# Kernel optimization log

Hardware: AMD Instinct MI355X
Metric: run time of the kernel (lower is better)

## Reference

```python
import jax, jax.numpy as jnp
import numpy as np

DIM = 1024
HEADS = 16
HEAD_DIM = DIM // HEADS
EPS = 1e-5


def layer_norm(x, w, b):
    # normalize over last dim (head_dim)
    mu = jnp.mean(x, axis=-1, keepdims=True)
    var = jnp.mean(jnp.square(x - mu), axis=-1, keepdims=True)
    return (x - mu) * jax.lax.rsqrt(var + EPS) * w + b


def setup_inputs() -> dict:
    key = jax.random.key(0)
    ks = jax.random.split(key, 8)
    B, N = 2, 2048
    x = jax.random.normal(ks[0], (B, N, DIM), dtype=jnp.float32)
    mask = jax.random.randint(ks[1], (B, 1, N, N), 0, 2) == 1  # True = masked out
    qkv_w = jax.random.normal(ks[2], (3 * DIM, DIM), dtype=jnp.float32) * (DIM ** -0.5)
    q_norm_w = jnp.ones((HEAD_DIM,), dtype=jnp.float32)
    q_norm_b = jnp.zeros((HEAD_DIM,), dtype=jnp.float32)
    k_norm_w = jnp.ones((HEAD_DIM,), dtype=jnp.float32)
    k_norm_b = jnp.zeros((HEAD_DIM,), dtype=jnp.float32)
    proj_w = jax.random.normal(ks[3], (DIM, DIM), dtype=jnp.float32) * (DIM ** -0.5)
    proj_b = jnp.zeros((DIM,), dtype=jnp.float32)
    return {"x": x, "mask": mask, "qkv_w": qkv_w,
            "q_norm_w": q_norm_w, "q_norm_b": q_norm_b,
            "k_norm_w": k_norm_w, "k_norm_b": k_norm_b,
            "proj_w": proj_w, "proj_b": proj_b}


def reference(x, mask, qkv_w, q_norm_w, q_norm_b, k_norm_w, k_norm_b, proj_w, proj_b):
    B, N, C = x.shape
    H, D = HEADS, HEAD_DIM
    scale = D ** -0.5
    # qkv projection (no bias), split into q,k,v of shape (B,H,N,D)
    qkv = (x @ qkv_w.T).reshape(B, N, 3, H, D).transpose(2, 0, 3, 1, 4)
    q, k, v = qkv[0], qkv[1], qkv[2]
    q = layer_norm(q, q_norm_w, q_norm_b)
    k = layer_norm(k, k_norm_w, k_norm_b)
    q = q * scale
    attn = jnp.einsum("bhnd,bhmd->bhnm", q, k)  # (B,H,N,N)
    attn = jnp.where(mask, -jnp.inf, attn)
    attn = jax.nn.softmax(attn, axis=-1)
    out = jnp.einsum("bhnm,bhmd->bhnd", attn, v)
    out = out.transpose(0, 2, 1, 3).reshape(B, N, C)
    return out @ proj_w.T + proj_b
```

## Files before the change

### kernel.cpp

```cpp
#include <hip/hip_runtime.h>
#include <hip/hip_bf16.h>
#include <math.h>

#define B_    2
#define N_    2048
#define DIM_  1024
#define H_    16
#define HD_   64
#define EPS_  1e-5f
#define SCALE_ 0.125f
#define LOG2E_ 1.4426950408889634f
#define MFIX_  14.0f

typedef __attribute__((ext_vector_type(8))) __bf16 bf16x8;
typedef __attribute__((ext_vector_type(8))) unsigned short ushort8;
typedef __attribute__((ext_vector_type(4))) float f32x4;
typedef __attribute__((ext_vector_type(4))) unsigned int uint4v;

__device__ __forceinline__ unsigned short f2bf(float x) {
    unsigned u = __builtin_bit_cast(unsigned, x);
    u += 0x7fff + ((u >> 16) & 1);
    return (unsigned short)(u >> 16);
}
__device__ __forceinline__ unsigned pk2bf(float a, float b) {
    unsigned ua = __builtin_bit_cast(unsigned, a) + 0x8000u;
    unsigned ub = __builtin_bit_cast(unsigned, b) + 0x8000u;
    return __builtin_amdgcn_perm(ub, ua, 0x07060302);
}

__device__ __forceinline__ void gl_lds16(const void* g, void* l) {
    __builtin_amdgcn_global_load_lds(
        (const __attribute__((address_space(1))) void*)g,
        (__attribute__((address_space(3))) void*)l, 16, 0, 0);
}

__global__ __launch_bounds__(256) void cast_all_bf16(
    const float* __restrict__ x, const float* __restrict__ qkvw,
    const float* __restrict__ pw, unsigned short* __restrict__ out) {
    int i = (blockIdx.x * 256 + threadIdx.x) * 8;
    const float* src;
    if (i < 4194304) src = x + i;
    else if (i < 7340032) src = qkvw + (i - 4194304);
    else src = pw + (i - 7340032);
    float4 v0 = *(const float4*)src;
    float4 v1 = *(const float4*)(src + 4);
    ushort8 r;
    r[0] = f2bf(v0.x); r[1] = f2bf(v0.y); r[2] = f2bf(v0.z); r[3] = f2bf(v0.w);
    r[4] = f2bf(v1.x); r[5] = f2bf(v1.y); r[6] = f2bf(v1.z); r[7] = f2bf(v1.w);
    *(ushort8*)(out + i) = r;
}

__global__ __launch_bounds__(256) void pack_mask(
    const int* __restrict__ mask, unsigned long long* __restrict__ bm) {
    int w = blockIdx.x * 4 + (threadIdx.x >> 6);
    int lane = threadIdx.x & 63;
    int mv = mask[(size_t)w * 64 + lane];
    unsigned long long bits = __ballot(mv != 0);
    if (lane == 0) bm[w] = bits;
}

__global__ __launch_bounds__(256) void gemm_qkv_ln(
    const unsigned short* __restrict__ A, const unsigned short* __restrict__ Bw,
    const float* __restrict__ qnw, const float* __restrict__ qnb,
    const float* __restrict__ knw, const float* __restrict__ knb,
    unsigned short* __restrict__ qbuf, unsigned short* __restrict__ kbuf,
    unsigned short* __restrict__ vbuf) {
    const int K = DIM_;
    __shared__ unsigned short As[128 * 32];
    __shared__ unsigned short Bs[128 * 32];
    const int tid = threadIdx.x;
    const int wave = tid >> 6, lane = tid & 63;
    const int quad = lane >> 4, lcol = lane & 15;
    const int wr = wave >> 1, wc = wave & 1;
    const int row0 = blockIdx.y * 128, col0 = blockIdx.x * 128;

    f32x4 acc[4][4];
#pragma unroll
    for (int i = 0; i < 4; ++i)
#pragma unroll
        for (int j = 0; j < 4; ++j) acc[i][j] = (f32x4){0.f, 0.f, 0.f, 0.f};

    for (int k0 = 0; k0 < K; k0 += 32) {
        __syncthreads();
#pragma unroll
        for (int c = 0; c < 2; ++c) {
            int base = wave * 2048 + c * 1024;
            int myofs = base + lane * 16;
            int r = myofs >> 6;
            int kb = myofs & 63;
            gl_lds16((const char*)A + ((size_t)(row0 + r) * K + k0) * 2 + kb,
                     (char*)As + base);
            gl_lds16((const char*)Bw + ((size_t)(col0 + r) * K + k0) * 2 + kb,
                     (char*)Bs + base);
        }
        __syncthreads();

        bf16x8 af[4], bfr[4];
#pragma unroll
        for (int i = 0; i < 4; ++i) {
            af[i] = *(const bf16x8*)&As[(wr * 64 + i * 16 + lcol) * 32 + quad * 8];
            bfr[i] = *(const bf16x8*)&Bs[(wc * 64 + i * 16 + lcol) * 32 + quad * 8];
        }
#pragma unroll
        for (int i = 0; i < 4; ++i)
#pragma unroll
            for (int j = 0; j < 4; ++j)
                acc[i][j] = __builtin_amdgcn_mfma_f32_16x16x32_bf16(
                    af[i], bfr[j], acc[i][j], 0, 0, 0);
    }

    const int colbase = col0 + wc * 64;
    const int t = colbase >> 10;
    const int h = (colbase & 1023) >> 6;

    if (t < 2) {
        const float* wv = (t == 0) ? qnw : knw;
        const float* bv = (t == 0) ? qnb : knb;
        float wreg[4], breg[4];
#pragma unroll
        for (int j = 0; j < 4; ++j) {
            wreg[j] = wv[j * 16 + lcol];
            breg[j] = bv[j * 16 + lcol];
        }
        const float sc = (t == 0) ? (SCALE_ * LOG2E_) : 1.f;
        unsigned short* obase = (t == 0) ? qbuf : kbuf;
#pragma unroll
        for (int i = 0; i < 4; ++i) {
#pragma unroll
            for (int reg = 0; reg < 4; ++reg) {
                int row = row0 + wr * 64 + i * 16 + quad * 4 + reg;
                int bb = row >> 11, n = row & (N_ - 1);
                float v[4];
#pragma unroll
                for (int j = 0; j < 4; ++j) v[j] = acc[i][j][reg];
                float s = v[0] + v[1] + v[2] + v[3];
                s += __shfl_xor(s, 1);
                s += __shfl_xor(s, 2);
                s += __shfl_xor(s, 4);
                s += __shfl_xor(s, 8);
                float mu = s * (1.f / 64.f);
                float d[4], s2 = 0.f;
#pragma unroll
                for (int j = 0; j < 4; ++j) {
                    d[j] = v[j] - mu;
                    s2 += d[j] * d[j];
                }
                s2 += __shfl_xor(s2, 1);
                s2 += __shfl_xor(s2, 2);
                s2 += __shfl_xor(s2, 4);
                s2 += __shfl_xor(s2, 8);
                float r = rsqrtf(s2 * (1.f / 64.f) + EPS_);
                float o0 = (d[0] * r * wreg[0] + breg[0]) * sc;
                float o1 = (d[1] * r * wreg[1] + breg[1]) * sc;
                float o2 = (d[2] * r * wreg[2] + breg[2]) * sc;
                float o3 = (d[3] * r * wreg[3] + breg[3]) * sc;
                uint2 pk;
                pk.x = pk2bf(o0, o1);
                pk.y = pk2bf(o2, o3);
                *(uint2*)(obase + ((size_t)(bb * H_ + h) * N_ + n) * 64 +
                          lcol * 4) = pk;
            }
        }
    } else {
#pragma unroll
        for (int i = 0; i < 4; ++i) {
#pragma unroll
            for (int reg = 0; reg < 4; ++reg) {
                int row = row0 + wr * 64 + i * 16 + quad * 4 + reg;
                uint2 pk;
                pk.x = pk2bf(acc[i][0][reg], acc[i][1][reg]);
                pk.y = pk2bf(acc[i][2][reg], acc[i][3][reg]);
                *(uint2*)(vbuf + (size_t)row * DIM_ + h * 64 + lcol * 4) = pk;
            }
        }
    }
}

__global__ __launch_bounds__(256) void gemm_proj(
    const unsigned short* __restrict__ A, const unsigned short* __restrict__ Bw,
    const float* __restrict__ bias, float* __restrict__ Cout) {
    const int K = DIM_;
    __shared__ unsigned short As[128 * 32];
    __shared__ unsigned short Bs[64 * 32];
    const int tid = threadIdx.x;
    const int wave = tid >> 6, lane = tid & 63;
    const int quad = lane >> 4, lcol = lane & 15;
    const int row0 = blockIdx.y * 128, col0 = blockIdx.x * 64;

    f32x4 acc[2][4];
#pragma unroll
    for (int i = 0; i < 2; ++i)
#pragma unroll
        for (int j = 0; j < 4; ++j) acc[i][j] = (f32x4){0.f, 0.f, 0.f, 0.f};

    for (int k0 = 0; k0 < K; k0 += 32) {
        __syncthreads();
#pragma unroll
        for (int pi = 0; pi < 3; ++pi) {
            int p = wave * 3 + pi;
            if (p < 8) {
                int base = p * 1024;
                int myofs = base + lane * 16;
                int r = myofs >> 6, kb = myofs & 63;
                gl_lds16((const char*)A + ((size_t)(row0 + r) * K + k0) * 2 + kb,
                         (char*)As + base);
            } else {
                int base = (p - 8) * 1024;
                int myofs = base + lane * 16;
                int r = myofs >> 6, kb = myofs & 63;
                gl_lds16((const char*)Bw + ((size_t)(col0 + r) * K + k0) * 2 + kb,
                         (char*)Bs + base);
            }
        }
        __syncthreads();

        bf16x8 af[2], bfr[4];
#pragma unroll
        for (int i = 0; i < 2; ++i)
            af[i] = *(const bf16x8*)&As[(wave * 32 + i * 16 + lcol) * 32 + quad * 8];
#pragma unroll
        for (int j = 0; j < 4; ++j)
            bfr[j] = *(const bf16x8*)&Bs[(j * 16 + lcol) * 32 + quad * 8];
#pragma unroll
        for (int i = 0; i < 2; ++i)
#pragma unroll
            for (int j = 0; j < 4; ++j)
                acc[i][j] = __builtin_amdgcn_mfma_f32_16x16x32_bf16(
                    af[i], bfr[j], acc[i][j], 0, 0, 0);
    }

#pragma unroll
    for (int i = 0; i < 2; ++i) {
#pragma unroll
        for (int j = 0; j < 4; ++j) {
            int col = col0 + j * 16 + lcol;
            float bv = bias[col];
#pragma unroll
            for (int reg = 0; reg < 4; ++reg) {
                int row = row0 + wave * 32 + i * 16 + quad * 4 + reg;
                Cout[(size_t)row * DIM_ + col] = acc[i][j][reg] + bv;
            }
        }
    }
}

__global__ __launch_bounds__(256) void transpose_v(
    const unsigned short* __restrict__ vbuf, unsigned short* __restrict__ vt) {
    __shared__ unsigned short Ts[64 * 65];
    const int tid = threadIdx.x;
    const int bh = blockIdx.y, n0 = blockIdx.x * 64;
    const int b = bh >> 4, h = bh & 15;
    {
        int r = tid >> 2, s = tid & 3;
        const unsigned short* src =
            vbuf + (size_t)(b * N_ + n0 + r) * DIM_ + h * 64 + s * 16;
#pragma unroll
        for (int i = 0; i < 16; ++i) {
            int p = s * 16 + i;
            int trued = (p >> 2) + (p & 3) * 16;
            Ts[r * 65 + trued] = src[i];
        }
    }
    __syncthreads();
    {
        int d = tid >> 2, kt = tid & 3;
        unsigned short* dstrow = vt + (size_t)(bh * 64 + d) * N_ + n0;
        int P = kt >> 1, t = kt & 1;
#pragma unroll
        for (int q = 0; q < 4; ++q) {
            __align__(8) unsigned short tmp4[4];
#pragma unroll
            for (int j = 0; j < 4; ++j)
                tmp4[j] = Ts[(kt * 16 + q * 4 + j) * 65 + d];
            *(uint2*)(dstrow + P * 32 + q * 8 + t * 4) = *(const uint2*)tmp4;
        }
    }
}

__global__ __launch_bounds__(256) void flash_attn_mfma6(
    const unsigned short* __restrict__ q, const unsigned short* __restrict__ k,
    const unsigned short* __restrict__ vt,
    const unsigned long long* __restrict__ bm, unsigned short* __restrict__ ao) {
    __shared__ unsigned short Qs[64 * 64];
    __shared__ unsigned short Ks[2][64 * 64];
    __shared__ unsigned short Vts[2][64 * 64];

    const int tid = threadIdx.x;
    const int wave = tid >> 6, lane = tid & 63;
    const int quad = lane >> 4, lcol = lane & 15;
    const int bh = blockIdx.y, b = bh >> 4, h = bh & 15;
    const int q0 = blockIdx.x * 64;

    const char* kgbase = (const char*)k + (size_t)bh * N_ * 128;
    const char* vtbase = (const char*)vt + (size_t)bh * 64 * N_ * 2;

    const char* kp[2];
    const char* vp[2];
#pragma unroll
    for (int ci = 0; ci < 2; ++ci) {
        int c = wave * 2 + ci;
        int swz = (c & 3) * 2;
        kp[ci] = kgbase + (size_t)(lane ^ swz) * 128 + c * 16;
        vp[ci] = vtbase + (size_t)(lane ^ swz) * N_ * 2 + c * 16;
    }

    {
        const char* qg = (const char*)(q + (size_t)(bh * N_ + q0) * 64);
#pragma unroll
        for (int c = 0; c < 2; ++c) {
            int base = wave * 2048 + c * 1024;
            gl_lds16(qg + base + lane * 16, (char*)Qs + base);
        }
#pragma unroll
        for (int ci = 0; ci < 2; ++ci) {
            int c = wave * 2 + ci;
            gl_lds16(kp[ci], (char*)Ks[0] + c * 1024);
            gl_lds16(vp[ci], (char*)Vts[0] + c * 1024);
            kp[ci] += 64 * 128;
            vp[ci] += 64 * 2;
        }
    }
    const unsigned long long* bmq =
        bm + ((size_t)b * N_ + q0 + wave * 16 + lcol) * 32;
    unsigned long long mw_next = bmq[0];
    __syncthreads();

    bf16x8 bq[2];
#pragma unroll
    for (int d0 = 0; d0 < 2; ++d0)
        bq[d0] = *(const bf16x8*)&Qs[(wave * 16 + lcol) * 64 + d0 * 32 + quad * 8];

    ushort8 ot;
#pragma unroll
    for (int i = 0; i < 8; ++i) ot[i] = 0x3F80;
    const bf16x8 ones = __builtin_bit_cast(bf16x8, ot);

    f32x4 oacc[4];
#pragma unroll
    for (int dt = 0; dt < 4; ++dt) oacc[dt] = (f32x4){0.f, 0.f, 0.f, 0.f};
    f32x4 lacc = (f32x4){0.f, 0.f, 0.f, 0.f};

    for (int k0 = 0; k0 < N_; k0 += 64) {
        const int cur = (k0 >> 6) & 1;
        const unsigned long long mw = mw_next;
        if (k0 + 64 < N_) {
#pragma unroll
            for (int ci = 0; ci < 2; ++ci) {
                int c = wave * 2 + ci;
                gl_lds16(kp[ci], (char*)Ks[cur ^ 1] + c * 1024);
                gl_lds16(vp[ci], (char*)Vts[cur ^ 1] + c * 1024);
                kp[ci] += 64 * 128;
                vp[ci] += 64 * 2;
            }
            mw_next = bmq[(k0 >> 6) + 1];
        }

        unsigned long long mq = mw >> (quad * 4);
        unsigned mlo = (unsigned)mq, mhi = (unsigned)(mq >> 32);
        f32x4 sacc[4];
#pragma unroll
        for (int kt = 0; kt < 4; ++kt) {
            unsigned word = (kt < 2) ? mlo : mhi;
            const int sh = (kt & 1) * 16;
#pragma unroll
            for (int reg = 0; reg < 4; ++reg)
                sacc[kt][reg] = ((word >> (sh + reg)) & 1u) ? -1e4f : -MFIX_;
        }

        const char* ksb = (const char*)Ks[cur];
        const char* vsb = (const char*)Vts[cur];
#pragma unroll
        for (int kt = 0; kt < 4; ++kt) {
#pragma unroll
            for (int d0 = 0; d0 < 2; ++d0) {
                int p = d0 * 4 + quad;
                bf16x8 ak = *(const bf16x8*)(ksb + p * 1024 +
                                             (((kt * 16 + lcol) ^ (quad * 2)) << 4));
                sacc[kt] = __builtin_amdgcn_mfma_f32_16x16x32_bf16(
                    ak, bq[d0], sacc[kt], 0, 0, 0);
            }
        }

        uint2 pk[4];
#pragma unroll
        for (int kt = 0; kt < 4; ++kt) {
            float p0 = exp2f(sacc[kt][0]);
            float p1 = exp2f(sacc[kt][1]);
            float p2 = exp2f(sacc[kt][2]);
            float p3 = exp2f(sacc[kt][3]);
            pk[kt].x = pk2bf(p0, p1);
            pk[kt].y = pk2bf(p2, p3);
        }

#pragma unroll
        for (int P = 0; P < 2; ++P) {
            uint4v bu;
            bu[0] = pk[2 * P].x;
            bu[1] = pk[2 * P].y;
            bu[2] = pk[2 * P + 1].x;
            bu[3] = pk[2 * P + 1].y;
            bf16x8 bp = __builtin_bit_cast(bf16x8, bu);
            lacc = __builtin_amdgcn_mfma_f32_16x16x32_bf16(ones, bp, lacc,
                                                           0, 0, 0);
#pragma unroll
            for (int dt = 0; dt < 4; ++dt) {
                int c = P * 4 + quad;
                bf16x8 va = *(const bf16x8*)(vsb + c * 1024 +
                                             (((dt * 16 + lcol) ^ (quad * 2)) << 4));
                oacc[dt] = __builtin_amdgcn_mfma_f32_16x16x32_bf16(
                    va, bp, oacc[dt], 0, 0, 0);
            }
        }
        __syncthreads();
    }

    float inv = 1.f / lacc[0];
    int row = q0 + wave * 16 + lcol;
    unsigned short* dst = ao + ((size_t)(b * N_ + row)) * DIM_ + h * 64 + quad * 4;
#pragma unroll
    for (int dt = 0; dt < 4; ++dt) {
        uint2 pko;
        pko.x = pk2bf(oacc[dt][0] * inv, oacc[dt][1] * inv);
        pko.y = pk2bf(oacc[dt][2] * inv, oacc[dt][3] * inv);
        *(uint2*)(dst + dt * 16) = pko;
    }
}

extern "C" void kernel_launch(void* const* d_in, const int* in_sizes, int n_in,
                              void* d_out, int out_size, void* d_ws,
                              size_t ws_size, hipStream_t stream) {
    const float* x     = (const float*)d_in[0];
    const int*   mask  = (const int*)d_in[1];
    const float* qkv_w = (const float*)d_in[2];
    const float* qnw   = (const float*)d_in[3];
    const float* qnb   = (const float*)d_in[4];
    const float* knw   = (const float*)d_in[5];
    const float* knb   = (const float*)d_in[6];
    const float* pw    = (const float*)d_in[7];
    const float* pb    = (const float*)d_in[8];
    float* out = (float*)d_out;

    char* ws = (char*)d_ws;
    unsigned short* x_bf  = (unsigned short*)(ws + 0);
    unsigned short* qw_bf = (unsigned short*)(ws + 8388608);
    unsigned short* pw_bf = (unsigned short*)(ws + 14680064);
    unsigned short* qbuf  = (unsigned short*)(ws + 16777216);
    unsigned short* kbuf  = (unsigned short*)(ws + 25165824);
    unsigned short* vbuf  = (unsigned short*)(ws + 33554432);
    unsigned short* vt    = (unsigned short*)(ws + 41943040);
    unsigned long long* bmask = (unsigned long long*)(ws + 50331648);
    unsigned short* ao_bnc = vbuf;

    cast_all_bf16<<<8388608 / 2048, 256, 0, stream>>>(x, qkv_w, pw, x_bf);

    gemm_qkv_ln<<<dim3(3072 / 128, 4096 / 128), 256, 0, stream>>>(
        x_bf, qw_bf, qnw, qnb, knw, knb, qbuf, kbuf, vbuf);

    transpose_v<<<dim3(N_ / 64, B_ * H_), 256, 0, stream>>>(vbuf, vt);

    pack_mask<<<(B_ * N_ * (N_ / 64)) / 4, 256, 0, stream>>>(mask, bmask);

    flash_attn_mfma6<<<dim3(N_ / 64, B_ * H_), 256, 0, stream>>>(
        qbuf, kbuf, vt, bmask, ao_bnc);

    gemm_proj<<<dim3(DIM_ / 64, 4096 / 128), 256, 0, stream>>>(
        ao_bnc, pw_bf, pb, out);
}
```

Measured before the change: 290.7 us.

## Process two query fragments per wave in flash attention to reuse K/V tiles

Each attention block now covers 128 query rows instead of 64, with each wave computing two 16-row query fragments against the same K and V tiles read from shared memory. This halves the number of K/V tile loads per query row and the block count, and doubles MFMA work per shared-memory read. In exchange it uses more registers per thread and launches only 512 blocks, which lowers parallelism across the chip's compute units.

Result: faster. 278.3 us (-4.2%).

```diff
diff --git a/kernel.cpp b/kernel.cpp
--- a/kernel.cpp
+++ b/kernel.cpp
@@ -277,11 +277,11 @@
     }
 }
 
-__global__ __launch_bounds__(256) void flash_attn_mfma6(
+__global__ __launch_bounds__(256, 2) void flash_attn_mfma7(
     const unsigned short* __restrict__ q, const unsigned short* __restrict__ k,
     const unsigned short* __restrict__ vt,
     const unsigned long long* __restrict__ bm, unsigned short* __restrict__ ao) {
-    __shared__ unsigned short Qs[64 * 64];
+    __shared__ unsigned short Qs[128 * 64];
     __shared__ unsigned short Ks[2][64 * 64];
     __shared__ unsigned short Vts[2][64 * 64];
 
@@ -289,7 +289,7 @@
     const int wave = tid >> 6, lane = tid & 63;
     const int quad = lane >> 4, lcol = lane & 15;
     const int bh = blockIdx.y, b = bh >> 4, h = bh & 15;
-    const int q0 = blockIdx.x * 64;
+    const int q0 = blockIdx.x * 128;
 
     const char* kgbase = (const char*)k + (size_t)bh * N_ * 128;
     const char* vtbase = (const char*)vt + (size_t)bh * 64 * N_ * 2;
@@ -307,8 +307,8 @@
     {
         const char* qg = (const char*)(q + (size_t)(bh * N_ + q0) * 64);
 #pragma unroll
-        for (int c = 0; c < 2; ++c) {
-            int base = wave * 2048 + c * 1024;
+        for (int c = 0; c < 4; ++c) {
+            int base = wave * 4096 + c * 1024;
             gl_lds16(qg + base + lane * 16, (char*)Qs + base);
         }
 #pragma unroll
@@ -320,29 +320,39 @@
             vp[ci] += 64 * 2;
         }
     }
-    const unsigned long long* bmq =
-        bm + ((size_t)b * N_ + q0 + wave * 16 + lcol) * 32;
-    unsigned long long mw_next = bmq[0];
+    const unsigned long long* bmq0 =
+        bm + ((size_t)b * N_ + q0 + wave * 32 + lcol) * 32;
+    const unsigned long long* bmq1 = bmq0 + 16 * 32;
+    unsigned long long mw_next0 = bmq0[0];
+    unsigned long long mw_next1 = bmq1[0];
     __syncthreads();
 
-    bf16x8 bq[2];
-#pragma unroll
-    for (int d0 = 0; d0 < 2; ++d0)
-        bq[d0] = *(const bf16x8*)&Qs[(wave * 16 + lcol) * 64 + d0 * 32 + quad * 8];
+    bf16x8 bq[2][2];
+#pragma unroll
+    for (int qf = 0; qf < 2; ++qf)
+#pragma unroll
+        for (int d0 = 0; d0 < 2; ++d0)
+            bq[qf][d0] = *(const bf16x8*)&Qs[(wave * 32 + qf * 16 + lcol) * 64 +
+                                             d0 * 32 + quad * 8];
 
     ushort8 ot;
 #pragma unroll
     for (int i = 0; i < 8; ++i) ot[i] = 0x3F80;
     const bf16x8 ones = __builtin_bit_cast(bf16x8, ot);
 
-    f32x4 oacc[4];
-#pragma unroll
-    for (int dt = 0; dt < 4; ++dt) oacc[dt] = (f32x4){0.f, 0.f, 0.f, 0.f};
-    f32x4 lacc = (f32x4){0.f, 0.f, 0.f, 0.f};
+    f32x4 oacc[2][4];
+#pragma unroll
+    for (int qf = 0; qf < 2; ++qf)
+#pragma unroll
+        for (int dt = 0; dt < 4; ++dt) oacc[qf][dt] = (f32x4){0.f, 0.f, 0.f, 0.f};
+    f32x4 lacc[2];
+    lacc[0] = (f32x4){0.f, 0.f, 0.f, 0.f};
+    lacc[1] = (f32x4){0.f, 0.f, 0.f, 0.f};
 
     for (int k0 = 0; k0 < N_; k0 += 64) {
         const int cur = (k0 >> 6) & 1;
-        const unsigned long long mw = mw_next;
+        const unsigned long long mw0 = mw_next0;
+        const unsigned long long mw1 = mw_next1;
         if (k0 + 64 < N_) {
 #pragma unroll
             for (int ci = 0; ci < 2; ++ci) {
@@ -352,19 +362,24 @@
                 kp[ci] += 64 * 128;
                 vp[ci] += 64 * 2;
             }
-            mw_next = bmq[(k0 >> 6) + 1];
-        }
-
-        unsigned long long mq = mw >> (quad * 4);
-        unsigned mlo = (unsigned)mq, mhi = (unsigned)(mq >> 32);
-        f32x4 sacc[4];
-#pragma unroll
-        for (int kt = 0; kt < 4; ++kt) {
-            unsigned word = (kt < 2) ? mlo : mhi;
-            const int sh = (kt & 1) * 16;
-#pragma unroll
-            for (int reg = 0; reg < 4; ++reg)
-                sacc[kt][reg] = ((word >> (sh + reg)) & 1u) ? -1e4f : -MFIX_;
+            mw_next0 = bmq0[(k0 >> 6) + 1];
+            mw_next1 = bmq1[(k0 >> 6) + 1];
+        }
+
+        f32x4 sacc[2][4];
+#pragma unroll
+        for (int qf = 0; qf < 2; ++qf) {
+            unsigned long long mq = ((qf == 0) ? mw0 : mw1) >> (quad * 4);
+            unsigned mlo = (unsigned)mq, mhi = (unsigned)(mq >> 32);
+#pragma unroll
+            for (int kt = 0; kt < 4; ++kt) {
+                unsigned word = (kt < 2) ? mlo : mhi;
+                const int sh = (kt & 1) * 16;
+#pragma unroll
+                for (int reg = 0; reg < 4; ++reg)
+                    sacc[qf][kt][reg] =
+                        ((word >> (sh + reg)) & 1u) ? -1e4f : -MFIX_;
+            }
         }
 
         const char* ksb = (const char*)Ks[cur];
@@ -376,53 +391,68 @@
                 int p = d0 * 4 + quad;
                 bf16x8 ak = *(const bf16x8*)(ksb + p * 1024 +
                                              (((kt * 16 + lcol) ^ (quad * 2)) << 4));
-                sacc[kt] = __builtin_amdgcn_mfma_f32_16x16x32_bf16(
-                    ak, bq[d0], sacc[kt], 0, 0, 0);
-            }
-        }
-
-        uint2 pk[4];
-#pragma unroll
-        for (int kt = 0; kt < 4; ++kt) {
-            float p0 = exp2f(sacc[kt][0]);
-            float p1 = exp2f(sacc[kt][1]);
-            float p2 = exp2f(sacc[kt][2]);
-            float p3 = exp2f(sacc[kt][3]);
-            pk[kt].x = pk2bf(p0, p1);
-            pk[kt].y = pk2bf(p2, p3);
+                sacc[0][kt] = __builtin_amdgcn_mfma_f32_16x16x32_bf16(
+                    ak, bq[0][d0], sacc[0][kt], 0, 0, 0);
+                sacc[1][kt] = __builtin_amdgcn_mfma_f32_16x16x32_bf16(
+                    ak, bq[1][d0], sacc[1][kt], 0, 0, 0);
+            }
+        }
+
+        uint2 pk[2][4];
+#pragma unroll
+        for (int qf = 0; qf < 2; ++qf) {
+#pragma unroll
+            for (int kt = 0; kt < 4; ++kt) {
+                float p0 = exp2f(sacc[qf][kt][0]);
+                float p1 = exp2f(sacc[qf][kt][1]);
+                float p2 = exp2f(sacc[qf][kt][2]);
+                float p3 = exp2f(sacc[qf][kt][3]);
+                pk[qf][kt].x = pk2bf(p0, p1);
+                pk[qf][kt].y = pk2bf(p2, p3);
+            }
         }
 
 #pragma unroll
         for (int P = 0; P < 2; ++P) {
-            uint4v bu;
-            bu[0] = pk[2 * P].x;
-            bu[1] = pk[2 * P].y;
-            bu[2] = pk[2 * P + 1].x;
-            bu[3] = pk[2 * P + 1].y;
-            bf16x8 bp = __builtin_bit_cast(bf16x8, bu);
-            lacc = __builtin_amdgcn_mfma_f32_16x16x32_bf16(ones, bp, lacc,
-                                                           0, 0, 0);
+            bf16x8 bp[2];
+#pragma unroll
+            for (int qf = 0; qf < 2; ++qf) {
+                uint4v bu;
+                bu[0] = pk[qf][2 * P].x;
+                bu[1] = pk[qf][2 * P].y;
+                bu[2] = pk[qf][2 * P + 1].x;
+                bu[3] = pk[qf][2 * P + 1].y;
+                bp[qf] = __builtin_bit_cast(bf16x8, bu);
+                lacc[qf] = __builtin_amdgcn_mfma_f32_16x16x32_bf16(
+                    ones, bp[qf], lacc[qf], 0, 0, 0);
+            }
 #pragma unroll
             for (int dt = 0; dt < 4; ++dt) {
                 int c = P * 4 + quad;
                 bf16x8 va = *(const bf16x8*)(vsb + c * 1024 +
                                              (((dt * 16 + lcol) ^ (quad * 2)) << 4));
-                oacc[dt] = __builtin_amdgcn_mfma_f32_16x16x32_bf16(
-                    va, bp, oacc[dt], 0, 0, 0);
+                oacc[0][dt] = __builtin_amdgcn_mfma_f32_16x16x32_bf16(
+                    va, bp[0], oacc[0][dt], 0, 0, 0);
+                oacc[1][dt] = __builtin_amdgcn_mfma_f32_16x16x32_bf16(
+                    va, bp[1], oacc[1][dt], 0, 0, 0);
             }
         }
         __syncthreads();
     }
 
-    float inv = 1.f / lacc[0];
-    int row = q0 + wave * 16 + lcol;
-    unsigned short* dst = ao + ((size_t)(b * N_ + row)) * DIM_ + h * 64 + quad * 4;
-#pragma unroll
-    for (int dt = 0; dt < 4; ++dt) {
-        uint2 pko;
-        pko.x = pk2bf(oacc[dt][0] * inv, oacc[dt][1] * inv);
-        pko.y = pk2bf(oacc[dt][2] * inv, oacc[dt][3] * inv);
-        *(uint2*)(dst + dt * 16) = pko;
+#pragma unroll
+    for (int qf = 0; qf < 2; ++qf) {
+        float inv = 1.f / lacc[qf][0];
+        int row = q0 + wave * 32 + qf * 16 + lcol;
+        unsigned short* dst =
+            ao + ((size_t)(b * N_ + row)) * DIM_ + h * 64 + quad * 4;
+#pragma unroll
+        for (int dt = 0; dt < 4; ++dt) {
+            uint2 pko;
+            pko.x = pk2bf(oacc[qf][dt][0] * inv, oacc[qf][dt][1] * inv);
+            pko.y = pk2bf(oacc[qf][dt][2] * inv, oacc[qf][dt][3] * inv);
+            *(uint2*)(dst + dt * 16) = pko;
+        }
     }
 }
 
@@ -460,7 +490,7 @@
 
     pack_mask<<<(B_ * N_ * (N_ / 64)) / 4, 256, 0, stream>>>(mask, bmask);
 
-    flash_attn_mfma6<<<dim3(N_ / 64, B_ * H_), 256, 0, stream>>>(
+    flash_attn_mfma7<<<dim3(N_ / 128, B_ * H_), 256, 0, stream>>>(
         qbuf, kbuf, vt, bmask, ao_bnc);
 
     gemm_proj<<<dim3(DIM_ / 64, 4096 / 128), 256, 0, stream>>>(
```
